# Optimization experiments

Measured on AMD Instinct MI355X. Metric: run time of the kernel, lower is better.

## Reference

```python
import jax, jax.numpy as jnp
import numpy as np

B, S, HID = 1, 2048, 2048
H, KVH, D = 16, 8, 128
N_REP = H // KVH
SCALING = float(np.sqrt(D))  # head_dim ** 0.5 (nGPT uses positive exponent)
SQK_INIT_VALUE = 1.0
SQK_INIT_SCALING = 0.02
EPS = 1e-8


def _rotate_half(x):
    x1, x2 = jnp.split(x, 2, axis=-1)
    return jnp.concatenate((-x2, x1), axis=-1)


def setup_inputs() -> dict:
    key = jax.random.key(0)
    ks = jax.random.split(key, 8)
    hidden_states = jax.random.normal(ks[0], (B, S, HID), dtype=jnp.float32)
    # realistic RoPE tables, full rotary (rotary_dim == head_dim)
    inv_freq = 1.0 / (10000.0 ** (np.arange(0, D, 2, dtype=np.float32) / D))
    t = np.arange(S, dtype=np.float32)
    freqs = np.outer(t, inv_freq)                      # [S, D/2]
    emb = np.concatenate([freqs, freqs], axis=-1)      # [S, D]
    cos = jnp.asarray(np.cos(emb))[None].repeat(B, 0)  # [B, S, D]
    sin = jnp.asarray(np.sin(emb))[None].repeat(B, 0)
    # additive causal mask [B, 1, S, S]
    causal = jnp.tril(jnp.ones((S, S), dtype=bool))
    attention_mask = jnp.where(causal, 0.0, jnp.finfo(jnp.float32).min)[None, None].repeat(B, 0)
    sd = 0.02
    Wq = jax.random.normal(ks[1], (H * D, HID), dtype=jnp.float32) * sd
    Wk = jax.random.normal(ks[2], (KVH * D, HID), dtype=jnp.float32) * sd
    Wv = jax.random.normal(ks[3], (KVH * D, HID), dtype=jnp.float32) * sd
    Wo = jax.random.normal(ks[4], (HID, H * D), dtype=jnp.float32) * sd
    sqk_w = jnp.full((H * D,), SQK_INIT_SCALING, dtype=jnp.float32)  # Linear(1, H*D) weight, init constant
    return {"hidden_states": hidden_states, "cos": cos, "sin": sin,
            "attention_mask": attention_mask, "Wq": Wq, "Wk": Wk, "Wv": Wv,
            "Wo": Wo, "sqk_w": sqk_w}


def _l2_normalize(x):
    return x / (jnp.linalg.norm(x, axis=-1, keepdims=True) + EPS)


def reference(hidden_states, cos, sin, attention_mask, Wq, Wk, Wv, Wo, sqk_w):
    b, s, _ = hidden_states.shape
    # projections (torch Linear: y = x @ W.T)
    q = jnp.einsum('bsd,ed->bse', hidden_states, Wq).reshape(b, s, H, D).transpose(0, 2, 1, 3)
    k = jnp.einsum('bsd,ed->bse', hidden_states, Wk).reshape(b, s, KVH, D).transpose(0, 2, 1, 3)
    v = jnp.einsum('bsd,ed->bse', hidden_states, Wv).reshape(b, s, KVH, D).transpose(0, 2, 1, 3)
    # RoPE, cos/sin broadcast over heads: [B,1,S,D]
    c, sn = cos[:, None], sin[:, None]
    q = q * c + _rotate_half(q) * sn
    k = k * c + _rotate_half(k) * sn
    # nGPT: L2-normalize q,k; learnable per-channel scale on q
    sqk = (sqk_w * (SQK_INIT_VALUE / SQK_INIT_SCALING)).reshape(1, H, 1, D)
    q = _l2_normalize(q) * sqk ** 2
    k = _l2_normalize(k)
    # GQA: repeat kv heads
    k = jnp.repeat(k, N_REP, axis=1)
    v = jnp.repeat(v, N_REP, axis=1)
    scores = jnp.einsum('bhqd,bhkd->bhqk', q, k) * SCALING
    scores = scores + attention_mask
    attn = jax.nn.softmax(scores.astype(jnp.float32), axis=-1).astype(q.dtype)
    out = jnp.einsum('bhqk,bhkd->bhqd', attn, v)
    out = out.transpose(0, 2, 1, 3).reshape(b, s, H * D)
    return jnp.einsum('bse,de->bsd', out, Wo)
```

## Files before the change

### kernel.cpp

```cpp
#include <hip/hip_runtime.h>

typedef unsigned short u16;
typedef __attribute__((ext_vector_type(4))) float f32x4;
typedef __attribute__((ext_vector_type(16))) float f32x16;
typedef __attribute__((ext_vector_type(8))) __bf16 bf16x8;
typedef __attribute__((ext_vector_type(8))) u16 u16x8;
typedef __attribute__((ext_vector_type(4))) u16 u16x4;
typedef __attribute__((ext_vector_type(4))) unsigned int u32x4;

#define S_LEN 2048
#define NH 16
#define NKV 8
#define QSCALE_LOG2E 16.322118857f
#define M2INIT 16.6f
#define EXP2(x) __builtin_amdgcn_exp2f(x)

#define SWZK(r) (((((r) & 7) << 4)) ^ (((((r) >> 3) & 1)) << 7))
#define SWZV(r) (((((r) & 7) << 4)) ^ (((((r) >> 3) & 1)) << 6))

#define AS1(p) ((const __attribute__((address_space(1))) void*)(p))
#define AS3(p) ((__attribute__((address_space(3))) void*)(p))

__device__ __forceinline__ float b2f(u16 u) {
    return __uint_as_float(((unsigned int)u) << 16);
}
__device__ __forceinline__ u16 f2b(float f) {
    unsigned int x = __float_as_uint(f);
    unsigned int r = (x + 0x7FFFu + ((x >> 16) & 1u)) >> 16;
    return (u16)r;
}

__global__ __launch_bounds__(256) void cast_all(const float* __restrict__ hs,
                                                const float* __restrict__ Wq,
                                                const float* __restrict__ Wk,
                                                const float* __restrict__ Wv,
                                                const float* __restrict__ Wo,
                                                u16* __restrict__ hsb,
                                                u16* __restrict__ wcat,
                                                u16* __restrict__ wob) {
    int i = blockIdx.x * 256 + threadIdx.x;
    const float* src; u16* dst; int off;
    if (i < 1048576)      { src = hs; dst = hsb;            off = i; }
    else if (i < 2097152) { src = Wq; dst = wcat;           off = i - 1048576; }
    else if (i < 2621440) { src = Wk; dst = wcat + 4194304; off = i - 2097152; }
    else if (i < 3145728) { src = Wv; dst = wcat + 6291456; off = i - 2621440; }
    else                  { src = Wo; dst = wob;            off = i - 3145728; }
    f32x4 v = reinterpret_cast<const f32x4*>(src)[off];
    u16x4 o;
    o[0] = f2b(v[0]); o[1] = f2b(v[1]); o[2] = f2b(v[2]); o[3] = f2b(v[3]);
    reinterpret_cast<u16x4*>(dst)[off] = o;
}

__global__ __launch_bounds__(256) void gemm_qkv(const u16* __restrict__ A,
                                                const u16* __restrict__ B,
                                                const float* __restrict__ cosb,
                                                const float* __restrict__ sinb,
                                                const float* __restrict__ sqkw,
                                                u16* __restrict__ qb,
                                                u16* __restrict__ kb,
                                                u16* __restrict__ vt) {
    const int K = 2048;
    __shared__ alignas(16) u16 As[2][128 * 64];
    __shared__ alignas(16) u16 Bs[2][128 * 64];
    int tid = threadIdx.x, lane = tid & 63, wave = tid >> 6;
    int row0 = blockIdx.y * 128, col0 = blockIdx.x * 128;
    int wr = wave * 32;
    int l15 = lane & 15, lg = lane >> 4;

    f32x4 acc[2][8] = {};

    auto stage = [&](int bf, int k0) {
#pragma unroll
        for (int i = 0; i < 4; i++) {
            int slot = i * 4 + wave;
            int r = slot * 8 + (lane >> 3);
            int c = lane & 7;
            __builtin_amdgcn_global_load_lds(AS1(A + (size_t)(row0 + r) * K + k0 + c * 8),
                                             AS3(&As[bf][slot * 512]), 16, 0, 0);
            __builtin_amdgcn_global_load_lds(AS1(B + (size_t)(col0 + r) * K + k0 + c * 8),
                                             AS3(&Bs[bf][slot * 512]), 16, 0, 0);
        }
    };

    stage(0, 0);
    __syncthreads();

    int nk = K >> 6, buf = 0;
    for (int t = 0; t < nk; ++t) {
        if (t + 1 < nk) stage(buf ^ 1, (t + 1) * 64);

        __builtin_amdgcn_s_setprio(1);
#pragma unroll
        for (int kk = 0; kk < 2; kk++) {
            bf16x8 af[2], bg[8];
#pragma unroll
            for (int m = 0; m < 2; m++)
                af[m] = *reinterpret_cast<const bf16x8*>(&As[buf][(wr + m * 16 + l15) * 64 + kk * 32 + lg * 8]);
#pragma unroll
            for (int n = 0; n < 8; n++)
                bg[n] = *reinterpret_cast<const bf16x8*>(&Bs[buf][(n * 16 + l15) * 64 + kk * 32 + lg * 8]);
#pragma unroll
            for (int m = 0; m < 2; m++)
#pragma unroll
                for (int n = 0; n < 8; n++)
                    acc[m][n] = __builtin_amdgcn_mfma_f32_16x16x32_bf16(af[m], bg[n], acc[m][n], 0, 0, 0);
        }
        __builtin_amdgcn_s_setprio(0);

        __syncthreads();
        buf ^= 1;
    }

    int bx = blockIdx.x;
    if (bx < 24) {
        bool isQ = bx < 16;
        float w2[8];
        if (isQ) {
#pragma unroll
            for (int j = 0; j < 8; j++) {
                float w = sqkw[bx * 128 + j * 16 + l15] * 50.f;
                w2[j] = w * w * QSCALE_LOG2E;
            }
        }
        u16* outb = isQ ? (qb + (size_t)bx * S_LEN * 128)
                        : (kb + (size_t)(bx - 16) * S_LEN * 128);
#pragma unroll
        for (int m = 0; m < 2; m++)
#pragma unroll
            for (int r = 0; r < 4; r++) {
                int s = row0 + wr + m * 16 + lg * 4 + r;
                const float* crow = cosb + (size_t)s * 128;
                const float* srow = sinb + (size_t)s * 128;
                float y[8];
                float ss = 0.f;
#pragma unroll
                for (int j = 0; j < 4; j++) {
                    float c  = crow[j * 16 + l15];
                    float sn = srow[j * 16 + l15];
                    float x0 = acc[m][j][r], x1 = acc[m][j + 4][r];
                    float a = x0 * c - x1 * sn;
                    float b = x1 * c + x0 * sn;
                    y[j] = a; y[j + 4] = b;
                    ss += a * a + b * b;
                }
                ss += __shfl_xor(ss, 1);
                ss += __shfl_xor(ss, 2);
                ss += __shfl_xor(ss, 4);
                ss += __shfl_xor(ss, 8);
                float inv = 1.f / (sqrtf(ss) + 1e-8f);
                u16* orow = outb + (size_t)s * 128;
                if (isQ) {
#pragma unroll
                    for (int j = 0; j < 8; j++)
                        orow[j * 16 + l15] = f2b(y[j] * inv * w2[j]);
                } else {
#pragma unroll
                    for (int j = 0; j < 8; j++)
                        orow[j * 16 + l15] = f2b(y[j] * inv);
                }
            }
    } else {
        int g = bx - 24;
#pragma unroll
        for (int n = 0; n < 8; n++) {
            int d = n * 16 + l15;
            u16* vrow = vt + (size_t)(g * 128 + d) * S_LEN;
#pragma unroll
            for (int m = 0; m < 2; m++) {
                u16x4 pk;
#pragma unroll
                for (int r = 0; r < 4; r++) pk[r] = f2b(acc[m][n][r]);
                *reinterpret_cast<u16x4*>(&vrow[row0 + wr + m * 16 + lg * 4]) = pk;
            }
        }
    }
}

template<int BM, int BN, int WM, int WN>
__global__ __launch_bounds__(256) void gemm_t(const u16* __restrict__ A,
                                              const u16* __restrict__ B,
                                              float* __restrict__ C,
                                              int M, int N, int K) {
    constexpr int MR = BM / WM / 16;
    constexpr int NR = BN / WN / 16;
    __shared__ alignas(16) u16 As[2][BM * 64];
    __shared__ alignas(16) u16 Bs[2][BN * 64];
    int tid = threadIdx.x, lane = tid & 63, wave = tid >> 6;
    int row0 = blockIdx.y * BM, col0 = blockIdx.x * BN;
    int wr = (wave / WN) * (BM / WM);
    int wc = (wave % WN) * (BN / WN);
    int l15 = lane & 15, lg = lane >> 4;

    f32x4 acc[MR][NR] = {};

    auto stage = [&](int bf, int k0) {
#pragma unroll
        for (int i = 0; i < BM / 32; i++) {
            int slot = i * 4 + wave;
            int r = slot * 8 + (lane >> 3);
            int c = lane & 7;
            __builtin_amdgcn_global_load_lds(AS1(A + (size_t)(row0 + r) * K + k0 + c * 8),
                                             AS3(&As[bf][slot * 512]), 16, 0, 0);
        }
#pragma unroll
        for (int i = 0; i < BN / 32; i++) {
            int slot = i * 4 + wave;
            int r = slot * 8 + (lane >> 3);
            int c = lane & 7;
            __builtin_amdgcn_global_load_lds(AS1(B + (size_t)(col0 + r) * K + k0 + c * 8),
                                             AS3(&Bs[bf][slot * 512]), 16, 0, 0);
        }
    };

    stage(0, 0);
    __syncthreads();

    int nk = K >> 6, buf = 0;
    for (int t = 0; t < nk; ++t) {
        if (t + 1 < nk) stage(buf ^ 1, (t + 1) * 64);

        __builtin_amdgcn_s_setprio(1);
#pragma unroll
        for (int kk = 0; kk < 2; kk++) {
            bf16x8 af[MR], bg[NR];
#pragma unroll
            for (int m = 0; m < MR; m++)
                af[m] = *reinterpret_cast<const bf16x8*>(&As[buf][(wr + m * 16 + l15) * 64 + kk * 32 + lg * 8]);
#pragma unroll
            for (int n = 0; n < NR; n++)
                bg[n] = *reinterpret_cast<const bf16x8*>(&Bs[buf][(wc + n * 16 + l15) * 64 + kk * 32 + lg * 8]);
#pragma unroll
            for (int m = 0; m < MR; m++)
#pragma unroll
                for (int n = 0; n < NR; n++)
                    acc[m][n] = __builtin_amdgcn_mfma_f32_16x16x32_bf16(af[m], bg[n], acc[m][n], 0, 0, 0);
        }
        __builtin_amdgcn_s_setprio(0);

        __syncthreads();
        buf ^= 1;
    }

#pragma unroll
    for (int m = 0; m < MR; m++)
#pragma unroll
        for (int n = 0; n < NR; n++)
#pragma unroll
            for (int r = 0; r < 4; r++) {
                int row = row0 + wr + m * 16 + lg * 4 + r;
                int col = col0 + wc + n * 16 + l15;
                C[(size_t)row * N + col] = acc[m][n][r];
            }
}

__global__ __launch_bounds__(256) void attn_mfma(const u16* __restrict__ Qb,
                                                 const u16* __restrict__ Kb,
                                                 const u16* __restrict__ Vt,
                                                 u16* __restrict__ Ao) {
    __shared__ alignas(16) char smem[50432];
    u16* Ks = (u16*)smem;
    u16* Vs = (u16*)(smem + 16384);
    float* scrO = (float*)smem;
    float* scrL = (float*)(smem + 32768);
    u16*   scrT = (u16*)(smem + 33024);

    int tid = threadIdx.x, lane = tid & 63, wv = tid >> 6;
    int h = blockIdx.x & (NH - 1);
    int z = blockIdx.x >> 4;
    int qi = (z < 16) ? (31 - z) : (z - 16);
    int qb0 = qi * 64;
    int g = h >> 1;
    int l31 = lane & 31, hi = lane >> 5;
    int qoff = (wv >> 1) * 32, koff = (wv & 1) * 32;
    int qabs = qb0 + qoff + l31;

    bf16x8 qf[8];
    {
        const u16* qrow = Qb + ((size_t)h * S_LEN + qabs) * 128;
#pragma unroll
        for (int kd = 0; kd < 8; kd++)
            qf[kd] = *reinterpret_cast<const bf16x8*>(qrow + kd * 16 + hi * 8);
    }

    const u16* kbase = Kb + (size_t)g * S_LEN * 128;
    const u16* vbase = Vt + (size_t)g * 128 * S_LEN;

    int rk = wv * 16 + (lane >> 4);
    int ck = lane & 15;
    int rv = wv * 32 + (lane >> 3);
    int cv = lane & 7;

    u16x8 kreg[4], vreg[4];
    f32x16 oacc[4] = {};
    float lpart = 0.f;

    int nt = qi + 1;

#pragma unroll
    for (int i = 0; i < 4; i++) {
        kreg[i] = *reinterpret_cast<const u16x8*>(kbase + (size_t)(rk + 4 * i) * 128 + ck * 8);
        vreg[i] = *reinterpret_cast<const u16x8*>(vbase + (size_t)(rv + 8 * i) * S_LEN + cv * 8);
    }

    for (int t = 0; t < nt; ++t) {
        int k0 = t * 64;
        __syncthreads();
#pragma unroll
        for (int i = 0; i < 4; i++) {
            int r = rk + 4 * i;
            *reinterpret_cast<u16x8*>((char*)Ks + r * 256 + ((ck * 16) ^ SWZK(r))) = kreg[i];
            int r2 = rv + 8 * i;
            *reinterpret_cast<u16x8*>((char*)Vs + r2 * 128 + ((cv * 16) ^ SWZV(r2))) = vreg[i];
        }
        __syncthreads();

        if (t + 1 < nt) {
            int kn = k0 + 64;
#pragma unroll
            for (int i = 0; i < 4; i++) {
                kreg[i] = *reinterpret_cast<const u16x8*>(kbase + (size_t)(kn + rk + 4 * i) * 128 + ck * 8);
                vreg[i] = *reinterpret_cast<const u16x8*>(vbase + (size_t)(rv + 8 * i) * S_LEN + kn + cv * 8);
            }
        }

        f32x16 s0 = {}, s1 = {};
        int krow = koff + l31;
        char* krp = (char*)Ks + krow * 256;
        int ksw = SWZK(krow);
        __builtin_amdgcn_s_setprio(1);
#pragma unroll
        for (int kd = 0; kd < 8; kd += 2) {
            bf16x8 kf0 = *reinterpret_cast<const bf16x8*>(krp + ((kd * 32 + hi * 16) ^ ksw));
            bf16x8 kf1 = *reinterpret_cast<const bf16x8*>(krp + (((kd + 1) * 32 + hi * 16) ^ ksw));
            s0 = __builtin_amdgcn_mfma_f32_32x32x16_bf16(kf0, qf[kd], s0, 0, 0, 0);
            s1 = __builtin_amdgcn_mfma_f32_32x32x16_bf16(kf1, qf[kd + 1], s1, 0, 0, 0);
        }
        __builtin_amdgcn_s_setprio(0);

        float p[16];
        bool maskt = (t == nt - 1);
#pragma unroll
        for (int r = 0; r < 16; r++) {
            float s = s0[r] + s1[r];
            if (maskt) {
                int key = k0 + koff + (r & 3) + 8 * (r >> 2) + 4 * hi;
                if (key > qabs) s = -1e30f;
            }
            float pv = EXP2(s - M2INIT);
            p[r] = pv;
            lpart += pv;
        }

        bf16x8 pf[2];
#pragma unroll
        for (int ks = 0; ks < 2; ks++) {
            int b = ks * 8;
            unsigned int A0 = (unsigned int)f2b(p[b + 0]) | ((unsigned int)f2b(p[b + 1]) << 16);
            unsigned int A1 = (unsigned int)f2b(p[b + 2]) | ((unsigned int)f2b(p[b + 3]) << 16);
            unsigned int A2 = (unsigned int)f2b(p[b + 4]) | ((unsigned int)f2b(p[b + 5]) << 16);
            unsigned int A3 = (unsigned int)f2b(p[b + 6]) | ((unsigned int)f2b(p[b + 7]) << 16);
            unsigned int S0 = __shfl_xor(A0, 32);
            unsigned int S1 = __shfl_xor(A1, 32);
            unsigned int S2 = __shfl_xor(A2, 32);
            unsigned int S3 = __shfl_xor(A3, 32);
            u32x4 w;
            w[0] = hi ? S2 : A0;
            w[1] = hi ? S3 : A1;
            w[2] = hi ? A2 : S0;
            w[3] = hi ? A3 : S1;
            pf[ks] = *reinterpret_cast<bf16x8*>(&w);
        }

        __builtin_amdgcn_s_setprio(1);
#pragma unroll
        for (int db = 0; db < 4; db++) {
            int vr = db * 32 + l31;
            char* vrp = (char*)Vs + vr * 128;
            int vsw = SWZV(vr);
#pragma unroll
            for (int ks = 0; ks < 2; ks++) {
                bf16x8 vf = *reinterpret_cast<const bf16x8*>(vrp + ((koff * 2 + ks * 32 + hi * 16) ^ vsw));
                oacc[db] = __builtin_amdgcn_mfma_f32_32x32x16_bf16(vf, pf[ks], oacc[db], 0, 0, 0);
            }
        }
        __builtin_amdgcn_s_setprio(0);
    }

    float lw = lpart + __shfl_xor(lpart, 32);
    int rg = wv >> 1;
    __syncthreads();
    if (wv & 1) {
#pragma unroll
        for (int db = 0; db < 4; db++)
#pragma unroll
            for (int r = 0; r < 16; r++) {
                int d = db * 32 + (r & 3) + 8 * (r >> 2) + 4 * hi;
                scrO[(rg * 128 + d) * 32 + l31] = oacc[db][r];
            }
        if (lane < 32) scrL[rg * 32 + l31] = lw;
    }
    __syncthreads();
    if (!(wv & 1)) {
        float inv = 1.f / (lw + scrL[rg * 32 + l31]);
#pragma unroll
        for (int db = 0; db < 4; db++)
#pragma unroll
            for (int r = 0; r < 16; r++) {
                int d = db * 32 + (r & 3) + 8 * (r >> 2) + 4 * hi;
                float o = (oacc[db][r] + scrO[(rg * 128 + d) * 32 + l31]) * inv;
                scrT[(rg * 32 + l31) * 136 + d] = f2b(o);
            }
    }
    __syncthreads();
    for (int i = tid; i < 64 * 16; i += 256) {
        int q = i >> 4, c = i & 15;
        u16x8 v = *reinterpret_cast<const u16x8*>(&scrT[q * 136 + c * 8]);
        *reinterpret_cast<u16x8*>(&Ao[(size_t)(qb0 + q) * 2048 + h * 128 + c * 8]) = v;
    }
}

extern "C" void kernel_launch(void* const* d_in, const int* in_sizes, int n_in,
                              void* d_out, int out_size, void* d_ws, size_t ws_size,
                              hipStream_t stream) {
    const float* hs   = (const float*)d_in[0];
    const float* cosb = (const float*)d_in[1];
    const float* sinb = (const float*)d_in[2];
    const float* Wq   = (const float*)d_in[4];
    const float* Wk   = (const float*)d_in[5];
    const float* Wv   = (const float*)d_in[6];
    const float* Wo   = (const float*)d_in[7];
    const float* sqkw = (const float*)d_in[8];

    char* ws = (char*)d_ws;
    u16*   hsb  = (u16*)(ws);
    u16*   wcat = (u16*)(ws + 8388608);
    u16*   wob  = (u16*)(ws + 25165824);
    u16*   qb   = (u16*)(ws + 33554432);
    u16*   kb   = (u16*)(ws + 41943040);
    u16*   vt   = (u16*)(ws + 46137344);
    u16*   ao   = (u16*)(ws + 50331648);

    cast_all<<<16384, 256, 0, stream>>>(hs, Wq, Wk, Wv, Wo, hsb, wcat, wob);

    gemm_qkv<<<dim3(32, 16), 256, 0, stream>>>(hsb, wcat, cosb, sinb, sqkw, qb, kb, vt);

    attn_mfma<<<512, 256, 0, stream>>>(qb, kb, vt, ao);

    gemm_t<128, 64, 4, 1><<<dim3(32, 16), 256, 0, stream>>>(ao, wob, (float*)d_out, 2048, 2048, 2048);
}
```

Before: 156.8 us.

## Triple-buffer QKV and output GEMMs with swizzled LDS and 512-thread tiles

```diff
diff --git a/kernel.cpp b/kernel.cpp
--- a/kernel.cpp
+++ b/kernel.cpp
@@ -20,6 +20,10 @@
 
 #define AS1(p) ((const __attribute__((address_space(1))) void*)(p))
 #define AS3(p) ((__attribute__((address_space(3))) void*)(p))
+
+#define PIPE_WAIT6() asm volatile("s_waitcnt vmcnt(6)\ns_barrier" ::: "memory")
+#define PIPE_WAIT4() asm volatile("s_waitcnt vmcnt(4)\ns_barrier" ::: "memory")
+#define PIPE_WAIT0() asm volatile("s_waitcnt vmcnt(0)\ns_barrier" ::: "memory")
 
 __device__ __forceinline__ float b2f(u16 u) {
     return __uint_as_float(((unsigned int)u) << 16);
@@ -51,7 +55,7 @@
     reinterpret_cast<u16x4*>(dst)[off] = o;
 }
 
-__global__ __launch_bounds__(256) void gemm_qkv(const u16* __restrict__ A,
+__global__ __launch_bounds__(512) void gemm_qkv(const u16* __restrict__ A,
                                                 const u16* __restrict__ B,
                                                 const float* __restrict__ cosb,
                                                 const float* __restrict__ sinb,
@@ -60,45 +64,59 @@
                                                 u16* __restrict__ kb,
                                                 u16* __restrict__ vt) {
     const int K = 2048;
-    __shared__ alignas(16) u16 As[2][128 * 64];
-    __shared__ alignas(16) u16 Bs[2][128 * 64];
+    __shared__ alignas(16) u16 As[3][128 * 64];
+    __shared__ alignas(16) u16 Bs[3][256 * 64];
     int tid = threadIdx.x, lane = tid & 63, wave = tid >> 6;
-    int row0 = blockIdx.y * 128, col0 = blockIdx.x * 128;
-    int wr = wave * 32;
+    int row0 = blockIdx.y * 128, col0 = blockIdx.x * 256;
+    int wr = (wave >> 1) * 32;
+    int wc = (wave & 1) * 128;
     int l15 = lane & 15, lg = lane >> 4;
 
     f32x4 acc[2][8] = {};
 
     auto stage = [&](int bf, int k0) {
 #pragma unroll
-        for (int i = 0; i < 4; i++) {
-            int slot = i * 4 + wave;
+        for (int i = 0; i < 2; i++) {
+            int slot = i * 8 + wave;
             int r = slot * 8 + (lane >> 3);
-            int c = lane & 7;
+            int c = (lane & 7) ^ (r & 7);
             __builtin_amdgcn_global_load_lds(AS1(A + (size_t)(row0 + r) * K + k0 + c * 8),
                                              AS3(&As[bf][slot * 512]), 16, 0, 0);
+        }
+#pragma unroll
+        for (int i = 0; i < 4; i++) {
+            int slot = i * 8 + wave;
+            int r = slot * 8 + (lane >> 3);
+            int c = (lane & 7) ^ (r & 7);
             __builtin_amdgcn_global_load_lds(AS1(B + (size_t)(col0 + r) * K + k0 + c * 8),
                                              AS3(&Bs[bf][slot * 512]), 16, 0, 0);
         }
     };
 
+    const int nk = K >> 6;
     stage(0, 0);
-    __syncthreads();
-
-    int nk = K >> 6, buf = 0;
+    stage(1, 64);
+
     for (int t = 0; t < nk; ++t) {
-        if (t + 1 < nk) stage(buf ^ 1, (t + 1) * 64);
+        int buf = t % 3;
+        __builtin_amdgcn_sched_barrier(0);
+        if (t + 1 < nk) PIPE_WAIT6(); else PIPE_WAIT0();
+        if (t + 2 < nk) stage((t + 2) % 3, (t + 2) * 64);
 
         __builtin_amdgcn_s_setprio(1);
 #pragma unroll
         for (int kk = 0; kk < 2; kk++) {
             bf16x8 af[2], bg[8];
 #pragma unroll
-            for (int m = 0; m < 2; m++)
-                af[m] = *reinterpret_cast<const bf16x8*>(&As[buf][(wr + m * 16 + l15) * 64 + kk * 32 + lg * 8]);
-#pragma unroll
-            for (int n = 0; n < 8; n++)
-                bg[n] = *reinterpret_cast<const bf16x8*>(&Bs[buf][(n * 16 + l15) * 64 + kk * 32 + lg * 8]);
+            for (int m = 0; m < 2; m++) {
+                int r = wr + m * 16 + l15;
+                af[m] = *reinterpret_cast<const bf16x8*>(&As[buf][r * 64 + (((kk * 4 + lg) ^ (r & 7)) * 8)]);
+            }
+#pragma unroll
+            for (int n = 0; n < 8; n++) {
+                int r = wc + n * 16 + l15;
+                bg[n] = *reinterpret_cast<const bf16x8*>(&Bs[buf][r * 64 + (((kk * 4 + lg) ^ (r & 7)) * 8)]);
+            }
 #pragma unroll
             for (int m = 0; m < 2; m++)
 #pragma unroll
@@ -106,24 +124,21 @@
                     acc[m][n] = __builtin_amdgcn_mfma_f32_16x16x32_bf16(af[m], bg[n], acc[m][n], 0, 0, 0);
         }
         __builtin_amdgcn_s_setprio(0);
-
-        __syncthreads();
-        buf ^= 1;
-    }
-
-    int bx = blockIdx.x;
-    if (bx < 24) {
-        bool isQ = bx < 16;
+    }
+
+    int c32 = blockIdx.x * 2 + (wave & 1);
+    if (c32 < 24) {
+        bool isQ = c32 < 16;
         float w2[8];
         if (isQ) {
 #pragma unroll
             for (int j = 0; j < 8; j++) {
-                float w = sqkw[bx * 128 + j * 16 + l15] * 50.f;
+                float w = sqkw[c32 * 128 + j * 16 + l15] * 50.f;
                 w2[j] = w * w * QSCALE_LOG2E;
             }
         }
-        u16* outb = isQ ? (qb + (size_t)bx * S_LEN * 128)
-                        : (kb + (size_t)(bx - 16) * S_LEN * 128);
+        u16* outb = isQ ? (qb + (size_t)c32 * S_LEN * 128)
+                        : (kb + (size_t)(c32 - 16) * S_LEN * 128);
 #pragma unroll
         for (int m = 0; m < 2; m++)
 #pragma unroll
@@ -160,7 +175,7 @@
                 }
             }
     } else {
-        int g = bx - 24;
+        int g = c32 - 24;
 #pragma unroll
         for (int n = 0; n < 8; n++) {
             int d = n * 16 + l15;
@@ -176,75 +191,76 @@
     }
 }
 
-template<int BM, int BN, int WM, int WN>
-__global__ __launch_bounds__(256) void gemm_t(const u16* __restrict__ A,
+__global__ __launch_bounds__(512) void gemm_o(const u16* __restrict__ A,
                                               const u16* __restrict__ B,
                                               float* __restrict__ C,
                                               int M, int N, int K) {
-    constexpr int MR = BM / WM / 16;
-    constexpr int NR = BN / WN / 16;
-    __shared__ alignas(16) u16 As[2][BM * 64];
-    __shared__ alignas(16) u16 Bs[2][BN * 64];
+    __shared__ alignas(16) u16 As[3][128 * 64];
+    __shared__ alignas(16) u16 Bs[3][128 * 64];
     int tid = threadIdx.x, lane = tid & 63, wave = tid >> 6;
-    int row0 = blockIdx.y * BM, col0 = blockIdx.x * BN;
-    int wr = (wave / WN) * (BM / WM);
-    int wc = (wave % WN) * (BN / WN);
+    int row0 = blockIdx.y * 128, col0 = blockIdx.x * 128;
+    int wr = (wave >> 1) * 32;
+    int wc = (wave & 1) * 64;
     int l15 = lane & 15, lg = lane >> 4;
 
-    f32x4 acc[MR][NR] = {};
+    f32x4 acc[2][4] = {};
 
     auto stage = [&](int bf, int k0) {
 #pragma unroll
-        for (int i = 0; i < BM / 32; i++) {
-            int slot = i * 4 + wave;
+        for (int i = 0; i < 2; i++) {
+            int slot = i * 8 + wave;
             int r = slot * 8 + (lane >> 3);
-            int c = lane & 7;
+            int c = (lane & 7) ^ (r & 7);
             __builtin_amdgcn_global_load_lds(AS1(A + (size_t)(row0 + r) * K + k0 + c * 8),
                                              AS3(&As[bf][slot * 512]), 16, 0, 0);
         }
 #pragma unroll
-        for (int i = 0; i < BN / 32; i++) {
-            int slot = i * 4 + wave;
+        for (int i = 0; i < 2; i++) {
+            int slot = i * 8 + wave;
             int r = slot * 8 + (lane >> 3);
-            int c = lane & 7;
+            int c = (lane & 7) ^ (r & 7);
             __builtin_amdgcn_global_load_lds(AS1(B + (size_t)(col0 + r) * K + k0 + c * 8),
                                              AS3(&Bs[bf][slot * 512]), 16, 0, 0);
         }
     };
 
+    const int nk = K >> 6;
     stage(0, 0);
-    __syncthreads();
-
-    int nk = K >> 6, buf = 0;
+    stage(1, 64);
+
     for (int t = 0; t < nk; ++t) {
-        if (t + 1 < nk) stage(buf ^ 1, (t + 1) * 64);
+        int buf = t % 3;
+        __builtin_amdgcn_sched_barrier(0);
+        if (t + 1 < nk) PIPE_WAIT4(); else PIPE_WAIT0();
+        if (t + 2 < nk) stage((t + 2) % 3, (t + 2) * 64);
 
         __builtin_amdgcn_s_setprio(1);
 #pragma unroll
         for (int kk = 0; kk < 2; kk++) {
-            bf16x8 af[MR], bg[NR];
-#pragma unroll
-            for (int m = 0; m < MR; m++)
-                af[m] = *reinterpret_cast<const bf16x8*>(&As[buf][(wr + m * 16 + l15) * 64 + kk * 32 + lg * 8]);
-#pragma unroll
-            for (int n = 0; n < NR; n++)
-                bg[n] = *reinterpret_cast<const bf16x8*>(&Bs[buf][(wc + n * 16 + l15) * 64 + kk * 32 + lg * 8]);
-#pragma unroll
-            for (int m = 0; m < MR; m++)
-#pragma unroll
-                for (int n = 0; n < NR; n++)
+            bf16x8 af[2], bg[4];
+#pragma unroll
+            for (int m = 0; m < 2; m++) {
+                int r = wr + m * 16 + l15;
+                af[m] = *reinterpret_cast<const bf16x8*>(&As[buf][r * 64 + (((kk * 4 + lg) ^ (r & 7)) * 8)]);
+            }
+#pragma unroll
+            for (int n = 0; n < 4; n++) {
+                int r = wc + n * 16 + l15;
+                bg[n] = *reinterpret_cast<const bf16x8*>(&Bs[buf][r * 64 + (((kk * 4 + lg) ^ (r & 7)) * 8)]);
+            }
+#pragma unroll
+            for (int m = 0; m < 2; m++)
+#pragma unroll
+                for (int n = 0; n < 4; n++)
                     acc[m][n] = __builtin_amdgcn_mfma_f32_16x16x32_bf16(af[m], bg[n], acc[m][n], 0, 0, 0);
         }
         __builtin_amdgcn_s_setprio(0);
-
-        __syncthreads();
-        buf ^= 1;
-    }
-
-#pragma unroll
-    for (int m = 0; m < MR; m++)
-#pragma unroll
-        for (int n = 0; n < NR; n++)
+    }
+
+#pragma unroll
+    for (int m = 0; m < 2; m++)
+#pragma unroll
+        for (int n = 0; n < 4; n++)
 #pragma unroll
             for (int r = 0; r < 4; r++) {
                 int row = row0 + wr + m * 16 + lg * 4 + r;
@@ -442,9 +458,9 @@
 
     cast_all<<<16384, 256, 0, stream>>>(hs, Wq, Wk, Wv, Wo, hsb, wcat, wob);
 
-    gemm_qkv<<<dim3(32, 16), 256, 0, stream>>>(hsb, wcat, cosb, sinb, sqkw, qb, kb, vt);
+    gemm_qkv<<<dim3(16, 16), 512, 0, stream>>>(hsb, wcat, cosb, sinb, sqkw, qb, kb, vt);
 
     attn_mfma<<<512, 256, 0, stream>>>(qb, kb, vt, ao);
 
-    gemm_t<128, 64, 4, 1><<<dim3(32, 16), 256, 0, stream>>>(ao, wob, (float*)d_out, 2048, 2048, 2048);
-}
+    gemm_o<<<dim3(16, 16), 512, 0, stream>>>(ao, wob, (float*)d_out, 2048, 2048, 2048);
+}
```

Result: faster. 148.7 us (-5.2%).
